# Optimization experiments

Measured on AMD Instinct MI355X. Metric: run time of the kernel, lower is better.

The kernel has to match this reference:

```python
import jax, jax.numpy as jnp
import numpy as np

NUM_NODES = 50000
NUM_EDGES = 800000
IN_F = 64
OUT_F = 64
EDGE_DIM = 16
NUM_GRAPHS = 64
T = 1.0
NEG_SLOPE = 0.2


def setup_inputs() -> dict:
    key = jax.random.key(0)
    k = jax.random.split(key, 6)
    x = jax.random.normal(k[0], (NUM_NODES, IN_F), dtype=jnp.float32)
    edge_index = jax.random.randint(k[1], (2, NUM_EDGES), 0, NUM_NODES, dtype=jnp.int32)
    edge_attr = jax.random.normal(k[2], (NUM_EDGES, EDGE_DIM), dtype=jnp.float32)
    batch_id = jnp.sort(jax.random.randint(k[3], (NUM_NODES,), 0, NUM_GRAPHS, dtype=jnp.int32))
    # Xavier-ish scaled params
    W = jax.random.normal(k[4], (IN_F, OUT_F), dtype=jnp.float32) * (1.0 / np.sqrt(IN_F))
    a = jax.random.normal(k[5], (2 * OUT_F + EDGE_DIM, 1), dtype=jnp.float32) * 0.1
    return {"x": x, "edge_index": edge_index, "edge_attr": edge_attr,
            "batch_id": batch_id, "W": W, "a": a}


def reference(x, edge_index, edge_attr, batch_id, W, a):
    num_nodes = x.shape[0]
    src0, dst0 = edge_index[0], edge_index[1]
    loop = jnp.arange(num_nodes, dtype=src0.dtype)
    # undirected: add reverse edges; then self loops
    src = jnp.concatenate([src0, dst0, loop])
    dst = jnp.concatenate([dst0, src0, loop])

    xt = x @ W  # [N, F]
    a_src = a[:OUT_F, 0]
    a_dst = a[OUT_F:2 * OUT_F, 0]
    a_edge = a[2 * OUT_F:, 0]
    # per-node attention contributions (equivalent to concat([h_src,h_dst,e]) @ a)
    s_node = xt @ a_src  # [N]
    d_node = xt @ a_dst  # [N]
    e_contrib = edge_attr @ a_edge  # [E]
    # self-loop edge_attr is zeros -> contribution 0
    e_all = jnp.concatenate([e_contrib, e_contrib, jnp.zeros((num_nodes,), xt.dtype)])

    logits = jax.nn.leaky_relu(s_node[src] + d_node[dst] + e_all, NEG_SLOPE) / T

    # segment softmax over dst
    m = jax.ops.segment_max(logits, dst, num_segments=num_nodes)
    z = jnp.exp(logits - m[dst])
    denom = jax.ops.segment_sum(z, dst, num_segments=num_nodes)
    att = z / denom[dst]  # [E_total]

    h_src = xt[src]  # [E_total, F]
    out = jax.ops.segment_sum(att[:, None] * h_src, dst, num_segments=num_nodes)
    return out
```

## Files before the change

### kernel.cpp

```cpp
#include <hip/hip_runtime.h>
#include <hip/hip_fp16.h>

#define N_NODES 50000
#define N_EDGES 800000
#define ETOT    (2 * N_EDGES + N_NODES)
#define F       64
#define NEG_SLOPE 0.2f
#define SCAN_B  1024
#define NB      ((N_NODES + SCAN_B - 1) / SCAN_B)

#define RSPLIT  4
#define NRANGE  (N_NODES / RSPLIT)
#define CCHUNK  64
#define EPC     (N_EDGES / CCHUNK)
#define BLD     1024

#define XT_TASKS (N_NODES / 16)

typedef _Float16 half8 __attribute__((ext_vector_type(8)));
typedef float    f32x4 __attribute__((ext_vector_type(4)));

__device__ __forceinline__ float leaky(float v) {
    return (v > 0.f) ? v : NEG_SLOPE * v;
}
__device__ __forceinline__ unsigned int pack_entry(int src, float w) {
    __half h = __float2half(w);
    return (unsigned int)(unsigned short)src |
           ((unsigned int)__half_as_ushort(h) << 16);
}

__global__ void __launch_bounds__(256) k_xt(const float* __restrict__ x,
                                            const float* __restrict__ W,
                                            const float* __restrict__ a,
                                            __half* __restrict__ xt,
                                            float2* __restrict__ sd) {
    const int lane = threadIdx.x & 63;
    const int task = blockIdx.x * 4 + (threadIdx.x >> 6);
    if (task >= XT_TASKS) return;
    const int n0  = task * 16;
    const int r16 = lane & 15;
    const int kb  = lane >> 4;

    half8 bf[4][2];
#pragma unroll
    for (int c = 0; c < 4; ++c)
#pragma unroll
        for (int ks = 0; ks < 2; ++ks) {
            const float* wp = W + (size_t)(ks * 32 + kb * 8) * 64 + c * 16 + r16;
#pragma unroll
            for (int j = 0; j < 8; ++j) bf[c][ks][j] = (_Float16)wp[j * 64];
        }

    half8 af[2];
#pragma unroll
    for (int ks = 0; ks < 2; ++ks) {
        const float* xp = x + (size_t)(n0 + r16) * F + ks * 32 + kb * 8;
        const float4 v0 = *(const float4*)xp;
        const float4 v1 = *(const float4*)(xp + 4);
        af[ks][0] = (_Float16)v0.x; af[ks][1] = (_Float16)v0.y;
        af[ks][2] = (_Float16)v0.z; af[ks][3] = (_Float16)v0.w;
        af[ks][4] = (_Float16)v1.x; af[ks][5] = (_Float16)v1.y;
        af[ks][6] = (_Float16)v1.z; af[ks][7] = (_Float16)v1.w;
    }

    f32x4 acc[4];
#pragma unroll
    for (int c = 0; c < 4; ++c) {
        acc[c] = (f32x4){0.f, 0.f, 0.f, 0.f};
        acc[c] = __builtin_amdgcn_mfma_f32_16x16x32_f16(af[0], bf[c][0], acc[c], 0, 0, 0);
        acc[c] = __builtin_amdgcn_mfma_f32_16x16x32_f16(af[1], bf[c][1], acc[c], 0, 0, 0);
    }

    float ps[4] = {0.f, 0.f, 0.f, 0.f};
    float pd[4] = {0.f, 0.f, 0.f, 0.f};
#pragma unroll
    for (int c = 0; c < 4; ++c) {
        const float as_ = a[c * 16 + r16];
        const float ad_ = a[64 + c * 16 + r16];
#pragma unroll
        for (int r = 0; r < 4; ++r) {
            const float v = acc[c][r];
            const int n = n0 + kb * 4 + r;
            xt[(size_t)n * F + c * 16 + r16] = __float2half(v);
            ps[r] = fmaf(v, as_, ps[r]);
            pd[r] = fmaf(v, ad_, pd[r]);
        }
    }
#pragma unroll
    for (int r = 0; r < 4; ++r) {
#pragma unroll
        for (int off = 1; off <= 8; off <<= 1) {
            ps[r] += __shfl_xor(ps[r], off);
            pd[r] += __shfl_xor(pd[r], off);
        }
    }
    if (r16 == 0) {
#pragma unroll
        for (int r = 0; r < 4; ++r) sd[n0 + kb * 4 + r] = make_float2(ps[r], pd[r]);
    }
}

__global__ void __launch_bounds__(BLD) k_histA(const int* __restrict__ srcs,
                                               const int* __restrict__ dsts,
                                               const float* __restrict__ ea,
                                               const float* __restrict__ a,
                                               float* __restrict__ ec,
                                               unsigned short* __restrict__ cnt) {
    __shared__ int h[NRANGE];
    const int c = blockIdx.x / RSPLIT, r = blockIdx.x % RSPLIT;
    const int nbase = r * NRANGE;
    for (int i = threadIdx.x; i < NRANGE; i += BLD) h[i] = 0;
    __syncthreads();
    const int e0 = c * EPC;
    for (int i = e0 + threadIdx.x; i < e0 + EPC; i += BLD) {
        const int d = dsts[i] - nbase;
        if ((unsigned)d < NRANGE) atomicAdd(&h[d], 1);
        const int s = srcs[i] - nbase;
        if ((unsigned)s < NRANGE) atomicAdd(&h[s], 1);
    }
    const int eq0 = e0 + (r * EPC) / RSPLIT;
    const int eq1 = e0 + ((r + 1) * EPC) / RSPLIT;
    for (int i = eq0 + threadIdx.x; i < eq1; i += BLD) {
        const float4* p = (const float4*)(ea + (size_t)i * 16);
        float acc = 0.f;
#pragma unroll
        for (int k = 0; k < 4; ++k) {
            float4 v = p[k];
            acc += v.x * a[128 + k * 4 + 0] + v.y * a[128 + k * 4 + 1] +
                   v.z * a[128 + k * 4 + 2] + v.w * a[128 + k * 4 + 3];
        }
        ec[i] = acc;
    }
    __syncthreads();
    unsigned short* o = cnt + (size_t)c * N_NODES + nbase;
    for (int i = threadIdx.x; i < NRANGE; i += BLD) o[i] = (unsigned short)h[i];
}

__global__ void k_scanA(unsigned short* __restrict__ cnt, int* __restrict__ part,
                        int* __restrict__ bsum) {
    __shared__ int wtot[16];
    __shared__ int wexc[16];
    const int tid = threadIdx.x, lane = tid & 63, wid = tid >> 6;
    const int i = blockIdx.x * SCAN_B + tid;
    int v = 0;
    if (i < N_NODES) {
        int run = 0;
#pragma unroll 8
        for (int c = 0; c < CCHUNK; ++c) {
            const int t = cnt[(size_t)c * N_NODES + i];
            cnt[(size_t)c * N_NODES + i] = (unsigned short)run;
            run += t;
        }
        v = run + 1;
    }
    int s = v;
#pragma unroll
    for (int off = 1; off < 64; off <<= 1) { int u = __shfl_up(s, off); if (lane >= off) s += u; }
    if (lane == 63) wtot[wid] = s;
    __syncthreads();
    if (tid == 0) { int run = 0; for (int w = 0; w < 16; ++w) { wexc[w] = run; run += wtot[w]; } bsum[blockIdx.x] = run; }
    __syncthreads();
    if (i < N_NODES) part[i] = wexc[wid] + s - v;
}

__global__ void k_scanB(int* __restrict__ bsum) {
    const int lane = threadIdx.x;
    const int v = (lane < NB) ? bsum[lane] : 0;
    int s = v;
#pragma unroll
    for (int off = 1; off < 64; off <<= 1) { int u = __shfl_up(s, off); if (lane >= off) s += u; }
    if (lane < NB) bsum[lane] = s - v;
}

__global__ void k_scanC(const int* __restrict__ part, const int* __restrict__ bsum,
                        const float2* __restrict__ sd, int* __restrict__ offs,
                        unsigned int* __restrict__ csr) {
    const int i = blockIdx.x * SCAN_B + threadIdx.x;
    if (i < N_NODES) {
        const int o = part[i] + bsum[blockIdx.x];
        offs[i] = o;
        const float2 v = sd[i];
        csr[o] = pack_entry(i, __expf(leaky(v.x + v.y)));
    }
    if (i == 0) offs[N_NODES] = ETOT;
}

__global__ void __launch_bounds__(BLD) k_scatter(const int* __restrict__ srcs,
                                                 const int* __restrict__ dsts,
                                                 const float2* __restrict__ sd,
                                                 const float* __restrict__ ec,
                                                 const unsigned short* __restrict__ cnt,
                                                 const int* __restrict__ offs,
                                                 unsigned int* __restrict__ csr) {
    __shared__ int cur[NRANGE];
    const int c = blockIdx.x / RSPLIT, r = blockIdx.x % RSPLIT;
    const int nbase = r * NRANGE;
    const unsigned short* cslice = cnt + (size_t)c * N_NODES + nbase;
    const int* oslice = offs + nbase;
    for (int i = threadIdx.x; i < NRANGE; i += BLD) cur[i] = oslice[i] + 1 + cslice[i];
    __syncthreads();
    const int e0 = c * EPC;
    for (int i = e0 + threadIdx.x; i < e0 + EPC; i += BLD) {
        const int s = srcs[i], d = dsts[i];
        const int dl = d - nbase, sl = s - nbase;
        const bool din = (unsigned)dl < NRANGE;
        const bool sin_ = (unsigned)sl < NRANGE;
        if (!din && !sin_) continue;
        const float e = ec[i];
        const float2 ss = sd[s], dd = sd[d];
        if (din) {
            const int pos = atomicAdd(&cur[dl], 1);
            csr[pos] = pack_entry(s, __expf(leaky(ss.x + dd.y + e)));
        }
        if (sin_) {
            const int pos = atomicAdd(&cur[sl], 1);
            csr[pos] = pack_entry(d, __expf(leaky(dd.x + ss.y + e)));
        }
    }
}

__global__ void __launch_bounds__(256) k_node(const int* __restrict__ offs,
                                              const unsigned int* __restrict__ csr,
                                              const __half* __restrict__ xt,
                                              float* __restrict__ out) {
    const int node = (blockIdx.x * blockDim.x + threadIdx.x) >> 6;
    const int lane = threadIdx.x & 63;
    if (node >= N_NODES) return;
    const int beg = offs[node], end = offs[node + 1];
    const int jg = lane >> 3;
    const int fc = lane & 7;
    float acc[8] = {0.f, 0.f, 0.f, 0.f, 0.f, 0.f, 0.f, 0.f};
    float sum = 0.f;
    for (int j = beg + jg; j < end; j += 8) {
        const unsigned int ent = csr[j];
        const int   src = (int)(ent & 0xFFFFu);
        const float w   = __half2float(__ushort_as_half((unsigned short)(ent >> 16)));
        sum += w;
        const uint4 hv = *(const uint4*)(xt + (size_t)src * F + fc * 8);
        const __half2* hp = (const __half2*)&hv;
#pragma unroll
        for (int k = 0; k < 4; ++k) {
            const float2 f = __half22float2(hp[k]);
            acc[2 * k]     += w * f.x;
            acc[2 * k + 1] += w * f.y;
        }
    }
#pragma unroll
    for (int off = 8; off <= 32; off <<= 1) {
        sum += __shfl_xor(sum, off);
#pragma unroll
        for (int k = 0; k < 8; ++k) acc[k] += __shfl_xor(acc[k], off);
    }
    if (jg == 0) {
        const float inv = 1.0f / sum;
        float4* op = (float4*)(out + (size_t)node * F + fc * 8);
        op[0] = make_float4(acc[0] * inv, acc[1] * inv, acc[2] * inv, acc[3] * inv);
        op[1] = make_float4(acc[4] * inv, acc[5] * inv, acc[6] * inv, acc[7] * inv);
    }
}

extern "C" void kernel_launch(void* const* d_in, const int* in_sizes, int n_in,
                              void* d_out, int out_size, void* d_ws, size_t ws_size,
                              hipStream_t stream) {
    const float* x    = (const float*)d_in[0];
    const int*   ei   = (const int*)d_in[1];
    const float* ea   = (const float*)d_in[2];
    const float* W    = (const float*)d_in[4];
    const float* a    = (const float*)d_in[5];
    float* out = (float*)d_out;

    const int* srcs = ei;
    const int* dsts = ei + N_EDGES;

    char* ws = (char*)d_ws;
    size_t off = 0;
    auto alloc = [&](size_t bytes) { void* p = ws + off; off = (off + bytes + 255) & ~(size_t)255; return p; };
    __half*         xt   = (__half*)alloc((size_t)N_NODES * F * 2);
    float2*         sd   = (float2*)alloc((size_t)N_NODES * 8);
    float*          ec   = (float*)alloc((size_t)N_EDGES * 4);
    unsigned short* cnt  = (unsigned short*)alloc((size_t)CCHUNK * N_NODES * 2);
    int*            part = (int*)alloc((size_t)N_NODES * 4);
    int*            bsum = (int*)alloc((size_t)NB * 4);
    int*            offs = (int*)alloc((size_t)(N_NODES + 1) * 4);
    unsigned int*   csr  = (unsigned int*)alloc((size_t)ETOT * 4);

    k_xt<<<(XT_TASKS + 3) / 4, 256, 0, stream>>>(x, W, a, xt, sd);
    k_histA<<<CCHUNK * RSPLIT, BLD, 0, stream>>>(srcs, dsts, ea, a, ec, cnt);
    k_scanA<<<NB, SCAN_B, 0, stream>>>(cnt, part, bsum);
    k_scanB<<<1, 64, 0, stream>>>(bsum);
    k_scanC<<<NB, SCAN_B, 0, stream>>>(part, bsum, sd, offs, csr);
    k_scatter<<<CCHUNK * RSPLIT, BLD, 0, stream>>>(srcs, dsts, sd, ec, cnt, offs, csr);
    k_node<<<((size_t)N_NODES * 64 + 255) / 256, 256, 0, stream>>>(offs, csr, xt, out);
}
```

Measured before the change: 109.3 us.

## Fold block-sum scan into scanC, remap block order, pack 8 nodes per wave in gather

The separate single-wave block-sum scan kernel is removed; each scanC block now rescans the block sums itself and takes its own base, saving one launch. Block index decoding for histogram and scatter interleaves chunk and range so neighbouring blocks cover different node ranges and adjacent chunks, which may change cache and LDS locality. The node gather kernel now gives each 8-lane group its own node and walks that node's edges serially, removing the cross-lane shuffle reduction. This costs load imbalance within a wave when degrees differ and less parallelism per node.

```diff
diff --git a/kernel.cpp b/kernel.cpp
--- a/kernel.cpp
+++ b/kernel.cpp
@@ -27,6 +27,11 @@
     __half h = __float2half(w);
     return (unsigned int)(unsigned short)src |
            ((unsigned int)__half_as_ushort(h) << 16);
+}
+__device__ __forceinline__ void cr_decode(int bid, int& c, int& r) {
+    const int m = bid & 7;
+    r = m >> 1;
+    c = ((bid >> 3) << 1) | (m & 1);
 }
 
 __global__ void __launch_bounds__(256) k_xt(const float* __restrict__ x,
@@ -107,7 +112,8 @@
                                                float* __restrict__ ec,
                                                unsigned short* __restrict__ cnt) {
     __shared__ int h[NRANGE];
-    const int c = blockIdx.x / RSPLIT, r = blockIdx.x % RSPLIT;
+    int c, r;
+    cr_decode(blockIdx.x, c, r);
     const int nbase = r * NRANGE;
     for (int i = threadIdx.x; i < NRANGE; i += BLD) h[i] = 0;
     __syncthreads();
@@ -163,21 +169,22 @@
     if (i < N_NODES) part[i] = wexc[wid] + s - v;
 }
 
-__global__ void k_scanB(int* __restrict__ bsum) {
-    const int lane = threadIdx.x;
-    const int v = (lane < NB) ? bsum[lane] : 0;
-    int s = v;
-#pragma unroll
-    for (int off = 1; off < 64; off <<= 1) { int u = __shfl_up(s, off); if (lane >= off) s += u; }
-    if (lane < NB) bsum[lane] = s - v;
-}
-
 __global__ void k_scanC(const int* __restrict__ part, const int* __restrict__ bsum,
                         const float2* __restrict__ sd, int* __restrict__ offs,
                         unsigned int* __restrict__ csr) {
+    __shared__ int base;
+    if (threadIdx.x < 64) {
+        const int lane = threadIdx.x;
+        const int v = (lane < NB) ? bsum[lane] : 0;
+        int s = v;
+#pragma unroll
+        for (int off = 1; off < 64; off <<= 1) { int u = __shfl_up(s, off); if (lane >= off) s += u; }
+        if (lane == (int)blockIdx.x) base = s - v;
+    }
+    __syncthreads();
     const int i = blockIdx.x * SCAN_B + threadIdx.x;
     if (i < N_NODES) {
-        const int o = part[i] + bsum[blockIdx.x];
+        const int o = part[i] + base;
         offs[i] = o;
         const float2 v = sd[i];
         csr[o] = pack_entry(i, __expf(leaky(v.x + v.y)));
@@ -193,7 +200,8 @@
                                                  const int* __restrict__ offs,
                                                  unsigned int* __restrict__ csr) {
     __shared__ int cur[NRANGE];
-    const int c = blockIdx.x / RSPLIT, r = blockIdx.x % RSPLIT;
+    int c, r;
+    cr_decode(blockIdx.x, c, r);
     const int nbase = r * NRANGE;
     const unsigned short* cslice = cnt + (size_t)c * N_NODES + nbase;
     const int* oslice = offs + nbase;
@@ -223,15 +231,16 @@
                                               const unsigned int* __restrict__ csr,
                                               const __half* __restrict__ xt,
                                               float* __restrict__ out) {
-    const int node = (blockIdx.x * blockDim.x + threadIdx.x) >> 6;
+    const int wid  = (blockIdx.x * blockDim.x + threadIdx.x) >> 6;
     const int lane = threadIdx.x & 63;
+    const int g    = lane >> 3;
+    const int fc   = lane & 7;
+    const int node = wid * 8 + g;
     if (node >= N_NODES) return;
     const int beg = offs[node], end = offs[node + 1];
-    const int jg = lane >> 3;
-    const int fc = lane & 7;
     float acc[8] = {0.f, 0.f, 0.f, 0.f, 0.f, 0.f, 0.f, 0.f};
     float sum = 0.f;
-    for (int j = beg + jg; j < end; j += 8) {
+    for (int j = beg; j < end; ++j) {
         const unsigned int ent = csr[j];
         const int   src = (int)(ent & 0xFFFFu);
         const float w   = __half2float(__ushort_as_half((unsigned short)(ent >> 16)));
@@ -245,18 +254,10 @@
             acc[2 * k + 1] += w * f.y;
         }
     }
-#pragma unroll
-    for (int off = 8; off <= 32; off <<= 1) {
-        sum += __shfl_xor(sum, off);
-#pragma unroll
-        for (int k = 0; k < 8; ++k) acc[k] += __shfl_xor(acc[k], off);
-    }
-    if (jg == 0) {
-        const float inv = 1.0f / sum;
-        float4* op = (float4*)(out + (size_t)node * F + fc * 8);
-        op[0] = make_float4(acc[0] * inv, acc[1] * inv, acc[2] * inv, acc[3] * inv);
-        op[1] = make_float4(acc[4] * inv, acc[5] * inv, acc[6] * inv, acc[7] * inv);
-    }
+    const float inv = 1.0f / sum;
+    float4* op = (float4*)(out + (size_t)node * F + fc * 8);
+    op[0] = make_float4(acc[0] * inv, acc[1] * inv, acc[2] * inv, acc[3] * inv);
+    op[1] = make_float4(acc[4] * inv, acc[5] * inv, acc[6] * inv, acc[7] * inv);
 }
 
 extern "C" void kernel_launch(void* const* d_in, const int* in_sizes, int n_in,
@@ -287,8 +288,7 @@
     k_xt<<<(XT_TASKS + 3) / 4, 256, 0, stream>>>(x, W, a, xt, sd);
     k_histA<<<CCHUNK * RSPLIT, BLD, 0, stream>>>(srcs, dsts, ea, a, ec, cnt);
     k_scanA<<<NB, SCAN_B, 0, stream>>>(cnt, part, bsum);
-    k_scanB<<<1, 64, 0, stream>>>(bsum);
     k_scanC<<<NB, SCAN_B, 0, stream>>>(part, bsum, sd, offs, csr);
     k_scatter<<<CCHUNK * RSPLIT, BLD, 0, stream>>>(srcs, dsts, sd, ec, cnt, offs, csr);
-    k_node<<<((size_t)N_NODES * 64 + 255) / 256, 256, 0, stream>>>(offs, csr, xt, out);
-}
+    k_node<<<((size_t)(N_NODES / 8) * 64 + 255) / 256, 256, 0, stream>>>(offs, csr, xt, out);
+}
```

Result: slower. 112.2 us (+2.6%).
